# Kernel tuning notes

Hardware: AMD Instinct MI355X
Metric: run time of the kernel (lower is better)

Reference implementation:

```python
import jax, jax.numpy as jnp
import numpy as np
from jax.scipy.special import logsumexp

PAD_IDX, SOS_IDX, EOS_IDX = 0, 1, 2
NEG = -10000.0


def setup_inputs() -> dict:
    B, T, L = 64, 256, 8
    K, E, H = 128, 256, 512      # num_tags, EMBED_SIZE, HIDDEN_SIZE
    CV, WV = 128, 50000          # char / word vocab
    key = jax.random.key(0)
    ks = jax.random.split(key, 12)
    lengths = jax.random.randint(ks[0], (B,), T // 2, T + 1)
    mask = jnp.arange(T)[None, :] < lengths[:, None]          # [B,T] contiguous prefix
    wx = jnp.where(mask, jax.random.randint(ks[1], (B, T), 3, WV), 0).astype(jnp.int32)
    cx = jax.random.randint(ks[2], (B, T, L), 0, CV).astype(jnp.int32)
    y_body = jnp.where(mask, jax.random.randint(ks[3], (B, T), 3, K), PAD_IDX)
    y = jnp.concatenate([jnp.full((B, 1), SOS_IDX, jnp.int32), y_body.astype(jnp.int32)], 1)  # [B,T+1]
    s = 0.05
    char_emb = s * jax.random.normal(ks[4], (CV, E), jnp.float32)
    word_emb = s * jax.random.normal(ks[5], (WV, E), jnp.float32)
    Wi = s * jax.random.normal(ks[6], (E, 4 * H), jnp.float32)
    Wh = s * jax.random.normal(ks[7], (H, 4 * H), jnp.float32)
    b = jnp.zeros((4 * H,), jnp.float32)
    Wout = s * jax.random.normal(ks[8], (H, K), jnp.float32)
    bout = jnp.zeros((K,), jnp.float32)
    trans = jax.random.normal(ks[9], (K, K), jnp.float32)
    trans = trans.at[SOS_IDX, :].set(NEG)
    trans = trans.at[:, EOS_IDX].set(NEG)
    trans = trans.at[:, PAD_IDX].set(NEG)
    trans = trans.at[PAD_IDX, :].set(NEG)
    trans = trans.at[PAD_IDX, EOS_IDX].set(0.0)
    trans = trans.at[PAD_IDX, PAD_IDX].set(0.0)
    return dict(cx=cx, wx=wx, y=y, char_emb=char_emb, word_emb=word_emb,
                Wi=Wi, Wh=Wh, b=b, Wout=Wout, bout=bout, trans=trans)


def _forward(cx, wx, y, char_emb, word_emb, Wi, Wh, b, Wout, bout, trans):
    B, T = wx.shape
    K = trans.shape[0]
    H = Wh.shape[0]
    mask = (wx > 0)                                            # [B,T] bool
    maskf = mask.astype(jnp.float32)
    # embedding: word lookup + mean-pooled char lookup
    x = word_emb[wx] + char_emb[cx].mean(axis=2)               # [B,T,E]

    # masked LSTM (equivalent to pack_padded for prefix masks)
    def lstm_step(carry, inp):
        h, c = carry
        xt, mt = inp                                            # [B,E], [B,1]
        z = xt @ Wi + h @ Wh + b                                # [B,4H]
        i, f, g, o = jnp.split(z, 4, axis=-1)
        i, f, o = jax.nn.sigmoid(i), jax.nn.sigmoid(f), jax.nn.sigmoid(o)
        c_new = f * c + i * jnp.tanh(g)
        h_new = o * jnp.tanh(c_new)
        h = jnp.where(mt, h_new, h)
        c = jnp.where(mt, c_new, c)
        return (h, c), h

    h0 = jnp.zeros((B, H), x.dtype)
    xs = jnp.swapaxes(x, 0, 1)                                  # [T,B,E]
    ms = jnp.swapaxes(mask, 0, 1)[..., None]                    # [T,B,1]
    _, hs = jax.lax.scan(lstm_step, (h0, h0), (xs, ms))         # [T,B,H]
    hs = jnp.swapaxes(hs, 0, 1)                                 # [B,T,H]
    h = (hs @ Wout + bout) * maskf[..., None]                   # emissions [B,T,K]

    # CRF forward algorithm (log partition Z)
    score0 = jnp.full((B, K), NEG, h.dtype).at[:, SOS_IDX].set(0.0)

    def crf_step(score, inp):
        em, mt = inp                                            # [B,K], [B,1]
        s_t = logsumexp(score[:, None, :] + em[:, :, None] + trans[None, :, :], axis=-1)
        return jnp.where(mt, s_t, score), None

    emT = jnp.swapaxes(h, 0, 1)                                 # [T,B,K]
    scoreZ, _ = jax.lax.scan(crf_step, score0, (emT, ms))
    Z = logsumexp(scoreZ + trans[EOS_IDX], axis=-1)             # [B]

    # gold path score
    y_prev, y_next = y[:, :-1], y[:, 1:]                        # [B,T]
    emit = jnp.take_along_axis(h, y_next[..., None], axis=-1)[..., 0]  # [B,T]
    tr = trans[y_next, y_prev]                                  # [B,T]
    gold = jnp.sum((emit + tr) * maskf, axis=1)                 # [B]
    lengths = mask.sum(axis=1)
    last_tag = y[jnp.arange(B), lengths]                        # y has T+1 cols
    gold = gold + trans[EOS_IDX, last_tag]
    return Z - gold                                             # NLL per sequence [B]


def reference(cx, wx, y, char_emb, word_emb, Wi, Wh, b, Wout, bout, trans):
    return _forward(cx, wx, y, char_emb, word_emb, Wi, Wh, b, Wout, bout, trans)
```

## Files before the change

kernel.cpp:

```cpp
#include <hip/hip_runtime.h>


typedef float f32x4 __attribute__((ext_vector_type(4)));
typedef float f32x16 __attribute__((ext_vector_type(16)));
typedef __bf16 bf16x8 __attribute__((ext_vector_type(8)));
typedef unsigned int u32x4 __attribute__((ext_vector_type(4)));
typedef unsigned int u32x2 __attribute__((ext_vector_type(2)));

#define T_LEN 256
#define BB    64
#define EE    256
#define HH    512
#define KK    128
#define KCAT  768

static __device__ inline unsigned f2bf(float f) {
  union { float f; unsigned u; } v; v.f = f;
  unsigned r = v.u + 0x7FFF + ((v.u >> 16) & 1);
  return r >> 16;
}
static __device__ inline float sigm(float x) { return 1.f / (1.f + __expf(-x)); }
static __device__ inline float tanh_fast(float x) {
  return 1.f - 2.f / (1.f + __expf(2.f * x));
}
static __device__ inline bf16x8 ubf(u32x4 v) {
  union { u32x4 u; bf16x8 b; } c; c.u = v; return c.b;
}

__global__ __launch_bounds__(256) void build_wcat(
    const float* __restrict__ Wi, const float* __restrict__ Wh,
    unsigned short* __restrict__ WcatT) {
  __shared__ float tile[64][65];
  int ct = blockIdx.x & 31, kt = blockIdx.x >> 5;
  int tc = threadIdx.x & 63, tr = threadIdx.x >> 6;
  int c0 = ct * 64, k0 = kt * 64;
#pragma unroll
  for (int i = 0; i < 16; ++i) {
    int r = tr * 16 + i, k = k0 + r;
    float v = (k < EE) ? Wi[(size_t)k * 2048 + c0 + tc]
                       : Wh[(size_t)(k - EE) * 2048 + c0 + tc];
    tile[r][tc] = v;
  }
  __syncthreads();
#pragma unroll
  for (int i = 0; i < 16; ++i) {
    int cL = tr * 16 + i;
    WcatT[(size_t)(c0 + cL) * KCAT + k0 + tc] = (unsigned short)f2bf(tile[tc][cL]);
  }
}

__global__ __launch_bounds__(256) void build_wout(
    const float* __restrict__ Wout, unsigned short* __restrict__ WoutT) {
  __shared__ float tile[64][65];
  int ct = blockIdx.x & 1, kt = blockIdx.x >> 1;
  int tc = threadIdx.x & 63, tr = threadIdx.x >> 6;
  int c0 = ct * 64, k0 = kt * 64;
#pragma unroll
  for (int i = 0; i < 16; ++i) {
    int r = tr * 16 + i;
    tile[r][tc] = Wout[(size_t)(k0 + r) * KK + c0 + tc];
  }
  __syncthreads();
#pragma unroll
  for (int i = 0; i < 16; ++i) {
    int cL = tr * 16 + i;
    WoutT[(size_t)(c0 + cL) * HH + k0 + tc] = (unsigned short)f2bf(tile[tc][cL]);
  }
}

__global__ __launch_bounds__(256) void embed_kernel(
    const int* __restrict__ wx, const int* __restrict__ cx,
    const float* __restrict__ we, const float* __restrict__ ce,
    unsigned short* __restrict__ x) {
  int bid = blockIdx.x;
  int t = bid >> 6, b = bid & 63;
  int e = threadIdx.x;
  int w = wx[b * T_LEN + t];
  float v = we[(size_t)w * EE + e];
  const int* cp = cx + ((size_t)(b * T_LEN + t)) * 8;
  float s = 0.f;
#pragma unroll
  for (int l = 0; l < 8; ++l) s += ce[(size_t)cp[l] * EE + e];
  v += s * 0.125f;
  x[(size_t)bid * EE + e] = (unsigned short)f2bf(v);
}

__global__ void zero_flags(unsigned int* __restrict__ f) {
  unsigned z = 0u;
  asm volatile("global_store_dword %0, %1, off sc0 sc1"
               :: "v"(f + threadIdx.x), "v"(z) : "memory");
}

#define SBAR __builtin_amdgcn_sched_barrier(0)
#define WAITV(N) do { asm volatile("s_waitcnt vmcnt(" #N ")" ::: "memory"); SBAR; } while (0)
#define LDC(dst, ptr, OFF) \
  asm volatile("global_load_dwordx4 %0, %1, off offset:" OFF " sc0 sc1" \
               : "=v"(dst) : "v"(ptr) : "memory")
#define LDN(dst, ptr, OFF) \
  asm volatile("global_load_dwordx4 %0, %1, off offset:" OFF \
               : "=v"(dst) : "v"(ptr) : "memory")

#define ISSUE_X(B, P) do { \
  LDN(B[0],P,"0");   LDN(B[1],P,"32");  LDN(B[2],P,"64");  LDN(B[3],P,"96"); \
  LDN(B[4],P,"128"); LDN(B[5],P,"160"); LDN(B[6],P,"192"); LDN(B[7],P,"224"); \
  LDN(B[8],P,"256"); LDN(B[9],P,"288"); LDN(B[10],P,"320"); LDN(B[11],P,"352"); \
  LDN(B[12],P,"384"); LDN(B[13],P,"416"); LDN(B[14],P,"448"); LDN(B[15],P,"480"); } while (0)
#define ISSUE_H0(B, P) do { \
  LDC(B[0],P,"0");   LDC(B[1],P,"32");  LDC(B[2],P,"64");  LDC(B[3],P,"96"); \
  LDC(B[4],P,"128"); LDC(B[5],P,"160"); LDC(B[6],P,"192"); LDC(B[7],P,"224"); \
  LDC(B[8],P,"256"); LDC(B[9],P,"288"); LDC(B[10],P,"320"); LDC(B[11],P,"352"); \
  LDC(B[12],P,"384"); LDC(B[13],P,"416"); LDC(B[14],P,"448"); LDC(B[15],P,"480"); } while (0)
#define ISSUE_H1(B, P) do { \
  LDC(B[0],P,"512"); LDC(B[1],P,"544"); LDC(B[2],P,"576"); LDC(B[3],P,"608"); \
  LDC(B[4],P,"640"); LDC(B[5],P,"672"); LDC(B[6],P,"704"); LDC(B[7],P,"736"); \
  LDC(B[8],P,"768"); LDC(B[9],P,"800"); LDC(B[10],P,"832"); LDC(B[11],P,"864"); \
  LDC(B[12],P,"896"); LDC(B[13],P,"928"); LDC(B[14],P,"960"); LDC(B[15],P,"992"); } while (0)

#define GATES_STORE(T) do { \
    bool mk = ((int)wxv) > 0; \
    _Pragma("unroll") \
    for (int r = 0; r < 4; ++r) { \
      float zi = acc[r], zf = acc[4 + r], zg = acc[8 + r], zo = acc[12 + r]; \
      float cn = sigm(zf) * cst[r] + sigm(zi) * tanh_fast(zg); \
      float hn = sigm(zo) * tanh_fast(cn); \
      if (mk) { cst[r] = cn; hst[r] = hn; } \
    } \
    u32x2 ph; \
    ph[0] = f2bf(hst[0]) | (f2bf(hst[1]) << 16); \
    ph[1] = f2bf(hst[2]) | (f2bf(hst[3]) << 16); \
    asm volatile("global_store_dwordx2 %0, %1, off sc0 sc1" \
                 :: "v"(hstore + (size_t)(T) * 65536), "v"(ph) : "memory"); \
  } while (0)

__global__ __launch_bounds__(128, 1) void lstm_persistent(
    const unsigned short* __restrict__ x,
    unsigned short* __restrict__ hs,
    const unsigned short* __restrict__ WcatT,
    const float* __restrict__ bias,
    const int* __restrict__ wx,
    unsigned int* __restrict__ flags) {
  const int tid = threadIdx.x;
  const int lane = tid & 63;
  const int bhalf = tid >> 6;
  const int hi = lane >> 5;
  const int batch = bhalf * 32 + (lane & 31);
  const int u0 = blockIdx.x * 8;
  const int rr = lane & 31;
  const int wcol = (rr >> 3) * HH + u0 + (rr & 7);

  bf16x8 wreg[48];
#pragma unroll
  for (int kf = 0; kf < 48; ++kf)
    wreg[kf] = *(const bf16x8*)(WcatT + (size_t)wcol * KCAT + kf * 16 + hi * 8);

  float bv[16];
#pragma unroll
  for (int q = 0; q < 4; ++q)
#pragma unroll
    for (int r = 0; r < 4; ++r)
      bv[q * 4 + r] = bias[q * HH + u0 + 4 * hi + r];

  const char* xlane  = (const char*)x  + ((size_t)batch * EE + hi * 8) * 2;
  const char* hread  = (const char*)hs + ((size_t)batch * HH + hi * 8) * 2;
  char*       hstore = (char*)hs + ((size_t)batch * HH + u0 + 4 * hi) * 2;
  const int*  wxp    = wx + batch * T_LEN;

  float cst[4] = {0.f, 0.f, 0.f, 0.f};
  float hst[4] = {0.f, 0.f, 0.f, 0.f};
  u32x4 bufX[16], bufH[16];
  unsigned wxv;
  f32x16 acc;

  ISSUE_X(bufX, xlane);
  asm volatile("global_load_dword %0, %1, off" : "=v"(wxv) : "v"(wxp) : "memory");
  WAITV(0);
#pragma unroll
  for (int i = 0; i < 16; ++i) acc[i] = bv[i];
#pragma unroll
  for (int kf = 0; kf < 16; ++kf)
    acc = __builtin_amdgcn_mfma_f32_32x32x16_bf16(wreg[kf], ubf(bufX[kf]), acc, 0, 0, 0);
  GATES_STORE(0);
  WAITV(0);
  __syncthreads();
  if (tid == 0)
    __hip_atomic_store(flags + blockIdx.x, 1u, __ATOMIC_RELAXED, __HIP_MEMORY_SCOPE_AGENT);

  for (int t = 1; t < T_LEN; ++t) {
    const char* xt = xlane + (size_t)t * 32768;
    const char* hp = hread + (size_t)(t - 1) * 65536;

    ISSUE_X(bufX, xt);
    asm volatile("global_load_dword %0, %1, off" : "=v"(wxv) : "v"(wxp + t) : "memory");
    {
      unsigned v;
      do {
        asm volatile("global_load_dword %0, %1, off sc0 sc1\n\ts_waitcnt vmcnt(0)"
                     : "=v"(v) : "v"(flags + lane) : "memory");
      } while (!__all((int)(v >= (unsigned)t)));
      SBAR;
    }
    ISSUE_H0(bufH, hp);
#pragma unroll
    for (int i = 0; i < 16; ++i) acc[i] = bv[i];
#pragma unroll
    for (int kf = 0; kf < 16; ++kf)
      acc = __builtin_amdgcn_mfma_f32_32x32x16_bf16(wreg[kf], ubf(bufX[kf]), acc, 0, 0, 0);
    SBAR;
    ISSUE_H1(bufX, hp);
    WAITV(16);
#pragma unroll
    for (int kf = 0; kf < 16; ++kf)
      acc = __builtin_amdgcn_mfma_f32_32x32x16_bf16(wreg[16 + kf], ubf(bufH[kf]), acc, 0, 0, 0);
    WAITV(0);
#pragma unroll
    for (int kf = 0; kf < 16; ++kf)
      acc = __builtin_amdgcn_mfma_f32_32x32x16_bf16(wreg[32 + kf], ubf(bufX[kf]), acc, 0, 0, 0);
    GATES_STORE(t);
    WAITV(0);
    __syncthreads();
    if (tid == 0)
      __hip_atomic_store(flags + blockIdx.x, (unsigned)(t + 1),
                         __ATOMIC_RELAXED, __HIP_MEMORY_SCOPE_AGENT);
  }
}

__global__ __launch_bounds__(512) void em_gemm(
    const unsigned short* __restrict__ hs,
    const unsigned short* __restrict__ WoutT,
    const float* __restrict__ bout,
    const int* __restrict__ wx,
    float* __restrict__ em) {
  int mg = blockIdx.x;
  int wave = threadIdx.x >> 6, lane = threadIdx.x & 63;
  int m = wave >> 1, nh = wave & 1;
  int arow = lane & 15, kg = (lane >> 4) * 8;
  int rbase = mg * 64 + m * 16;
  const unsigned short* A = hs + (size_t)(rbase + arow) * HH + kg;
  f32x4 acc[4];
#pragma unroll
  for (int nt = 0; nt < 4; ++nt) acc[nt] = (f32x4){0.f, 0.f, 0.f, 0.f};
#pragma unroll
  for (int ks = 0; ks < 16; ++ks) {
    bf16x8 a = *(const bf16x8*)(A + ks * 32);
#pragma unroll
    for (int nt = 0; nt < 4; ++nt) {
      const unsigned short* Bp =
          WoutT + (size_t)(nh * 64 + nt * 16 + arow) * HH + kg + ks * 32;
      acc[nt] = __builtin_amdgcn_mfma_f32_16x16x32_bf16(a, *(const bf16x8*)Bp, acc[nt], 0, 0, 0);
    }
  }
#pragma unroll
  for (int nt = 0; nt < 4; ++nt) {
    int n = nh * 64 + nt * 16 + arow;
    float bo = bout[n];
#pragma unroll
    for (int r = 0; r < 4; ++r) {
      int row = rbase + (lane >> 4) * 4 + r;
      int t = row >> 6, b = row & 63;
      float v = (acc[nt][r] + bo) * ((wx[b * T_LEN + t] > 0) ? 1.f : 0.f);
      em[(size_t)row * KK + n] = v;
    }
  }
}

__global__ __launch_bounds__(512) void crf_kernel(
    const float* __restrict__ em,
    const float* __restrict__ trans,
    const int* __restrict__ wx,
    const int* __restrict__ y,
    float* __restrict__ out) {
  int b = blockIdx.x;
  __shared__ float tl[KK][129];
  __shared__ float sc[KK];
  __shared__ float red[512];
  __shared__ float red2[512];
  int tid = threadIdx.x;
  for (int i = tid; i < KK * KK; i += 512) tl[i >> 7][i & 127] = trans[i];
  if (tid < KK) sc[tid] = (tid == 1) ? 0.f : -10000.f;
  __syncthreads();

  int k = tid & 127, q = tid >> 7, j0 = q * 32;

  for (int t = 0; t < T_LEN; ++t) {
    if (wx[b * T_LEN + t] <= 0) continue;
    float mx = -1e30f;
#pragma unroll
    for (int j = 0; j < 32; ++j) mx = fmaxf(mx, sc[j0 + j] + tl[k][j0 + j]);
    float s = 0.f;
#pragma unroll
    for (int j = 0; j < 32; ++j) s += __expf(sc[j0 + j] + tl[k][j0 + j] - mx);
    red[tid] = mx; red2[tid] = s;
    __syncthreads();
    if (q == 0) {
      float M = mx, S = s;
#pragma unroll
      for (int qq = 1; qq < 4; ++qq) {
        float m2 = red[qq * 128 + k], s2 = red2[qq * 128 + k];
        float Mn = fmaxf(M, m2);
        S = S * __expf(M - Mn) + s2 * __expf(m2 - Mn);
        M = Mn;
      }
      sc[k] = em[(size_t)(t * BB + b) * KK + k] + M + __logf(S);
    }
    __syncthreads();
  }

  float term = 0.f, cnt = 0.f;
  if (tid < T_LEN) {
    int yp = y[b * 257 + tid], yn = y[b * 257 + tid + 1];
    if (wx[b * T_LEN + tid] > 0) {
      term = em[(size_t)(tid * BB + b) * KK + yn] + tl[yn][yp];
      cnt = 1.f;
    }
  }
  red[tid] = term; red2[tid] = cnt;
  __syncthreads();
  for (int s2 = 256; s2 > 0; s2 >>= 1) {
    if (tid < s2) { red[tid] += red[tid + s2]; red2[tid] += red2[tid + s2]; }
    __syncthreads();
  }
  float gold = red[0];
  int len = (int)(red2[0] + 0.5f);
  __syncthreads();

  float v = (tid < KK) ? sc[tid] + tl[2][tid] : -3.0e38f;
  red[tid] = v;
  __syncthreads();
  for (int s2 = 256; s2 > 0; s2 >>= 1) {
    if (tid < s2) red[tid] = fmaxf(red[tid], red[tid + s2]);
    __syncthreads();
  }
  float mz = red[0];
  __syncthreads();
  red[tid] = (tid < KK) ? __expf(v - mz) : 0.f;
  __syncthreads();
  for (int s2 = 256; s2 > 0; s2 >>= 1) {
    if (tid < s2) red[tid] += red[tid + s2];
    __syncthreads();
  }
  if (tid == 0) {
    float Z = mz + __logf(red[0]);
    int last_tag = y[b * 257 + len];
    out[b] = Z - (gold + tl[2][last_tag]);
  }
}

extern "C" void kernel_launch(void* const* d_in, const int* in_sizes, int n_in,
                              void* d_out, int out_size, void* d_ws, size_t ws_size,
                              hipStream_t stream) {
  const int*   cx    = (const int*)d_in[0];
  const int*   wx    = (const int*)d_in[1];
  const int*   y     = (const int*)d_in[2];
  const float* ce    = (const float*)d_in[3];
  const float* we    = (const float*)d_in[4];
  const float* Wi    = (const float*)d_in[5];
  const float* Wh    = (const float*)d_in[6];
  const float* bias  = (const float*)d_in[7];
  const float* Wout  = (const float*)d_in[8];
  const float* bout  = (const float*)d_in[9];
  const float* trans = (const float*)d_in[10];
  float* out = (float*)d_out;

  char* ws = (char*)d_ws;
  unsigned short* WcatT = (unsigned short*)(ws + 0);
  unsigned short* WoutT = (unsigned short*)(ws + 3145728);
  unsigned short* x     = (unsigned short*)(ws + 3276800);
  unsigned short* hs    = (unsigned short*)(ws + 11665408);
  unsigned int*   flags = (unsigned int*)(ws + 28442624);
  float*          em    = (float*)(ws + 3276800);

  build_wcat<<<384, 256, 0, stream>>>(Wi, Wh, WcatT);
  build_wout<<<16, 256, 0, stream>>>(Wout, WoutT);
  embed_kernel<<<T_LEN * BB, 256, 0, stream>>>(wx, cx, we, ce, x);
  zero_flags<<<1, 64, 0, stream>>>(flags);
  lstm_persistent<<<64, 128, 0, stream>>>(x, hs, WcatT, bias, wx, flags);
  em_gemm<<<256, 512, 0, stream>>>(hs, WoutT, bout, wx, em);
  crf_kernel<<<BB, 512, 0, stream>>>(em, trans, wx, y, out);
}
```

Baseline: 1.757 ms.

## Stream LSTM weights per step instead of register-resident, pad flags, precompute masks

The persistent LSTM kernel no longer keeps all 48 weight fragments in registers. It reloads them from global memory (L2) every timestep in 8-fragment double-buffered chunks, interleaved with the x and h loads and the MFMAs. Per-block flags are padded to separate 64-byte slots, only wave 0 polls (with s_sleep and an iteration cap), and the mask bits are precomputed into bitmasks. This relieves register pressure and polling contention, but adds per-step weight traffic on the serial critical path, and the poll cap could let a block proceed before the others are ready.

```diff
diff --git a/kernel.cpp b/kernel.cpp
--- a/kernel.cpp
+++ b/kernel.cpp
@@ -4,7 +4,6 @@
 typedef float f32x4 __attribute__((ext_vector_type(4)));
 typedef float f32x16 __attribute__((ext_vector_type(16)));
 typedef __bf16 bf16x8 __attribute__((ext_vector_type(8)));
-typedef unsigned int u32x4 __attribute__((ext_vector_type(4)));
 typedef unsigned int u32x2 __attribute__((ext_vector_type(2)));
 
 #define T_LEN 256
@@ -22,9 +21,6 @@
 static __device__ inline float sigm(float x) { return 1.f / (1.f + __expf(-x)); }
 static __device__ inline float tanh_fast(float x) {
   return 1.f - 2.f / (1.f + __expf(2.f * x));
-}
-static __device__ inline bf16x8 ubf(u32x4 v) {
-  union { u32x4 u; bf16x8 b; } c; c.u = v; return c.b;
 }
 
 __global__ __launch_bounds__(256) void build_wcat(
@@ -88,48 +84,29 @@
 __global__ void zero_flags(unsigned int* __restrict__ f) {
   unsigned z = 0u;
   asm volatile("global_store_dword %0, %1, off sc0 sc1"
-               :: "v"(f + threadIdx.x), "v"(z) : "memory");
+               :: "v"(f + blockIdx.x * 256 + threadIdx.x), "v"(z) : "memory");
 }
 
 #define SBAR __builtin_amdgcn_sched_barrier(0)
 #define WAITV(N) do { asm volatile("s_waitcnt vmcnt(" #N ")" ::: "memory"); SBAR; } while (0)
-#define LDC(dst, ptr, OFF) \
+#define LD(dst, p, OFF) \
+  asm volatile("global_load_dwordx4 %0, %1, off offset:" OFF \
+               : "=v"(dst) : "v"(p) : "memory")
+#define LS(dst, p, OFF) \
   asm volatile("global_load_dwordx4 %0, %1, off offset:" OFF " sc0 sc1" \
-               : "=v"(dst) : "v"(ptr) : "memory")
-#define LDN(dst, ptr, OFF) \
-  asm volatile("global_load_dwordx4 %0, %1, off offset:" OFF \
-               : "=v"(dst) : "v"(ptr) : "memory")
-
-#define ISSUE_X(B, P) do { \
-  LDN(B[0],P,"0");   LDN(B[1],P,"32");  LDN(B[2],P,"64");  LDN(B[3],P,"96"); \
-  LDN(B[4],P,"128"); LDN(B[5],P,"160"); LDN(B[6],P,"192"); LDN(B[7],P,"224"); \
-  LDN(B[8],P,"256"); LDN(B[9],P,"288"); LDN(B[10],P,"320"); LDN(B[11],P,"352"); \
-  LDN(B[12],P,"384"); LDN(B[13],P,"416"); LDN(B[14],P,"448"); LDN(B[15],P,"480"); } while (0)
-#define ISSUE_H0(B, P) do { \
-  LDC(B[0],P,"0");   LDC(B[1],P,"32");  LDC(B[2],P,"64");  LDC(B[3],P,"96"); \
-  LDC(B[4],P,"128"); LDC(B[5],P,"160"); LDC(B[6],P,"192"); LDC(B[7],P,"224"); \
-  LDC(B[8],P,"256"); LDC(B[9],P,"288"); LDC(B[10],P,"320"); LDC(B[11],P,"352"); \
-  LDC(B[12],P,"384"); LDC(B[13],P,"416"); LDC(B[14],P,"448"); LDC(B[15],P,"480"); } while (0)
-#define ISSUE_H1(B, P) do { \
-  LDC(B[0],P,"512"); LDC(B[1],P,"544"); LDC(B[2],P,"576"); LDC(B[3],P,"608"); \
-  LDC(B[4],P,"640"); LDC(B[5],P,"672"); LDC(B[6],P,"704"); LDC(B[7],P,"736"); \
-  LDC(B[8],P,"768"); LDC(B[9],P,"800"); LDC(B[10],P,"832"); LDC(B[11],P,"864"); \
-  LDC(B[12],P,"896"); LDC(B[13],P,"928"); LDC(B[14],P,"960"); LDC(B[15],P,"992"); } while (0)
-
-#define GATES_STORE(T) do { \
-    bool mk = ((int)wxv) > 0; \
-    _Pragma("unroll") \
-    for (int r = 0; r < 4; ++r) { \
-      float zi = acc[r], zf = acc[4 + r], zg = acc[8 + r], zo = acc[12 + r]; \
-      float cn = sigm(zf) * cst[r] + sigm(zi) * tanh_fast(zg); \
-      float hn = sigm(zo) * tanh_fast(cn); \
-      if (mk) { cst[r] = cn; hst[r] = hn; } \
-    } \
-    u32x2 ph; \
-    ph[0] = f2bf(hst[0]) | (f2bf(hst[1]) << 16); \
-    ph[1] = f2bf(hst[2]) | (f2bf(hst[3]) << 16); \
-    asm volatile("global_store_dwordx2 %0, %1, off sc0 sc1" \
-                 :: "v"(hstore + (size_t)(T) * 65536), "v"(ph) : "memory"); \
+               : "=v"(dst) : "v"(p) : "memory")
+
+#define IS_P8(B, P) do { \
+  LD(B[0],P,"0");   LD(B[1],P,"32");  LD(B[2],P,"64");  LD(B[3],P,"96"); \
+  LD(B[4],P,"128"); LD(B[5],P,"160"); LD(B[6],P,"192"); LD(B[7],P,"224"); } while (0)
+#define IS_S8(B, P) do { \
+  LS(B[0],P,"0");   LS(B[1],P,"32");  LS(B[2],P,"64");  LS(B[3],P,"96"); \
+  LS(B[4],P,"128"); LS(B[5],P,"160"); LS(B[6],P,"192"); LS(B[7],P,"224"); } while (0)
+
+#define MFMA8(W, D) do { \
+  _Pragma("unroll") \
+  for (int j_ = 0; j_ < 8; ++j_) \
+    acc = __builtin_amdgcn_mfma_f32_32x32x16_bf16(W[j_], D[j_], acc, 0, 0, 0); \
   } while (0)
 
 __global__ __launch_bounds__(128, 1) void lstm_persistent(
@@ -140,87 +117,103 @@
     const int* __restrict__ wx,
     unsigned int* __restrict__ flags) {
   const int tid = threadIdx.x;
-  const int lane = tid & 63;
-  const int bhalf = tid >> 6;
-  const int hi = lane >> 5;
-  const int batch = bhalf * 32 + (lane & 31);
+  const int wave = tid >> 6, lane = tid & 63;
+  const int hi2 = lane >> 5;
+  const int batch = wave * 32 + (lane & 31);
   const int u0 = blockIdx.x * 8;
   const int rr = lane & 31;
-  const int wcol = (rr >> 3) * HH + u0 + (rr & 7);
-
-  bf16x8 wreg[48];
-#pragma unroll
-  for (int kf = 0; kf < 48; ++kf)
-    wreg[kf] = *(const bf16x8*)(WcatT + (size_t)wcol * KCAT + kf * 16 + hi * 8);
+  const int col = (rr >> 3) * HH + u0 + (rr & 7);
+
+  const char* wbase = (const char*)WcatT + ((size_t)col * KCAT + hi2 * 8) * 2;
+  const char* xp    = (const char*)x + ((size_t)batch * EE + hi2 * 8) * 2;
+  const char* hp    = (const char*)hs + ((size_t)batch * HH + hi2 * 8) * 2;
+  char*       hstp  = (char*)hs + ((size_t)batch * HH + u0 + 4 * hi2) * 2;
+  unsigned int* myflag = flags + blockIdx.x * 16;
 
   float bv[16];
 #pragma unroll
-  for (int q = 0; q < 4; ++q)
-#pragma unroll
-    for (int r = 0; r < 4; ++r)
-      bv[q * 4 + r] = bias[q * HH + u0 + 4 * hi + r];
-
-  const char* xlane  = (const char*)x  + ((size_t)batch * EE + hi * 8) * 2;
-  const char* hread  = (const char*)hs + ((size_t)batch * HH + hi * 8) * 2;
-  char*       hstore = (char*)hs + ((size_t)batch * HH + u0 + 4 * hi) * 2;
-  const int*  wxp    = wx + batch * T_LEN;
-
-  float cst[4] = {0.f, 0.f, 0.f, 0.f};
-  float hst[4] = {0.f, 0.f, 0.f, 0.f};
-  u32x4 bufX[16], bufH[16];
-  unsigned wxv;
+  for (int g = 0; g < 4; ++g)
+#pragma unroll
+    for (int j = 0; j < 4; ++j) bv[g * 4 + j] = bias[g * HH + u0 + 4 * hi2 + j];
+
+  const int* wxp = wx + batch * T_LEN;
+  unsigned m8[8];
+#pragma unroll
+  for (int w8 = 0; w8 < 8; ++w8) {
+    unsigned m = 0;
+#pragma unroll
+    for (int k2 = 0; k2 < 32; ++k2)
+      m |= (wxp[w8 * 32 + k2] > 0) ? (1u << k2) : 0u;
+    m8[w8] = m;
+  }
+
+  float cst[4] = {0.f, 0.f, 0.f, 0.f}, hst[4] = {0.f, 0.f, 0.f, 0.f};
+  bf16x8 WA[8], DA[8], WB[8], DB[8];
   f32x16 acc;
 
-  ISSUE_X(bufX, xlane);
-  asm volatile("global_load_dword %0, %1, off" : "=v"(wxv) : "v"(wxp) : "memory");
-  WAITV(0);
-#pragma unroll
-  for (int i = 0; i < 16; ++i) acc[i] = bv[i];
-#pragma unroll
-  for (int kf = 0; kf < 16; ++kf)
-    acc = __builtin_amdgcn_mfma_f32_32x32x16_bf16(wreg[kf], ubf(bufX[kf]), acc, 0, 0, 0);
-  GATES_STORE(0);
-  WAITV(0);
-  __syncthreads();
-  if (tid == 0)
-    __hip_atomic_store(flags + blockIdx.x, 1u, __ATOMIC_RELAXED, __HIP_MEMORY_SCOPE_AGENT);
-
-  for (int t = 1; t < T_LEN; ++t) {
-    const char* xt = xlane + (size_t)t * 32768;
-    const char* hp = hread + (size_t)(t - 1) * 65536;
-
-    ISSUE_X(bufX, xt);
-    asm volatile("global_load_dword %0, %1, off" : "=v"(wxv) : "v"(wxp + t) : "memory");
-    {
-      unsigned v;
-      do {
-        asm volatile("global_load_dword %0, %1, off sc0 sc1\n\ts_waitcnt vmcnt(0)"
-                     : "=v"(v) : "v"(flags + lane) : "memory");
-      } while (!__all((int)(v >= (unsigned)t)));
-      SBAR;
-    }
-    ISSUE_H0(bufH, hp);
-#pragma unroll
-    for (int i = 0; i < 16; ++i) acc[i] = bv[i];
-#pragma unroll
-    for (int kf = 0; kf < 16; ++kf)
-      acc = __builtin_amdgcn_mfma_f32_32x32x16_bf16(wreg[kf], ubf(bufX[kf]), acc, 0, 0, 0);
-    SBAR;
-    ISSUE_H1(bufX, hp);
-    WAITV(16);
-#pragma unroll
-    for (int kf = 0; kf < 16; ++kf)
-      acc = __builtin_amdgcn_mfma_f32_32x32x16_bf16(wreg[16 + kf], ubf(bufH[kf]), acc, 0, 0, 0);
-    WAITV(0);
-#pragma unroll
-    for (int kf = 0; kf < 16; ++kf)
-      acc = __builtin_amdgcn_mfma_f32_32x32x16_bf16(wreg[32 + kf], ubf(bufX[kf]), acc, 0, 0, 0);
-    GATES_STORE(t);
-    WAITV(0);
-    __syncthreads();
-    if (tid == 0)
-      __hip_atomic_store(flags + blockIdx.x, (unsigned)(t + 1),
-                         __ATOMIC_RELAXED, __HIP_MEMORY_SCOPE_AGENT);
+#pragma unroll
+  for (int ph = 0; ph < 8; ++ph) {
+    const unsigned mw = m8[ph];
+#pragma unroll 1
+    for (int tt = 0; tt < 32; ++tt) {
+      const int t = ph * 32 + tt;
+      const bool mk = (mw >> tt) & 1u;
+
+      if (t > 0) {
+        if (wave == 0) {
+          unsigned v_; int it_ = 0;
+          for (;;) {
+            asm volatile("global_load_dword %0, %1, off sc0 sc1\n\ts_waitcnt vmcnt(0)"
+                         : "=v"(v_) : "v"(flags + lane * 16) : "memory");
+            if (__all((int)(v_ >= (unsigned)t))) break;
+            if (++it_ >= 65536) break;
+            __builtin_amdgcn_s_sleep(1);
+          }
+          SBAR;
+        }
+        __syncthreads();
+      }
+
+      const char* xt = xp + (size_t)t * 32768;
+      const char* ht = hp + (size_t)(t - 1) * 65536;
+
+      IS_P8(WA, wbase);         IS_P8(DA, xt);
+      IS_P8(WB, (wbase + 256)); IS_P8(DB, (xt + 256));
+#pragma unroll
+      for (int i = 0; i < 16; ++i) acc[i] = bv[i];
+      WAITV(16);  MFMA8(WA, DA);
+      if (t > 0) {
+        IS_P8(WA, (wbase + 512));  IS_S8(DA, ht);
+        WAITV(16);  MFMA8(WB, DB);
+        IS_P8(WB, (wbase + 768));  IS_S8(DB, (ht + 256));
+        WAITV(16);  MFMA8(WA, DA);
+        IS_P8(WA, (wbase + 1024)); IS_S8(DA, (ht + 512));
+        WAITV(16);  MFMA8(WB, DB);
+        IS_P8(WB, (wbase + 1280)); IS_S8(DB, (ht + 768));
+        WAITV(16);  MFMA8(WA, DA);
+        WAITV(0);   MFMA8(WB, DB);
+      } else {
+        WAITV(0);   MFMA8(WB, DB);
+      }
+
+#pragma unroll
+      for (int r = 0; r < 4; ++r) {
+        float zi = acc[r], zf = acc[4 + r], zg = acc[8 + r], zo = acc[12 + r];
+        float cn = sigm(zf) * cst[r] + sigm(zi) * tanh_fast(zg);
+        float hn = sigm(zo) * tanh_fast(cn);
+        if (mk) { cst[r] = cn; hst[r] = hn; }
+      }
+      u32x2 phh;
+      phh[0] = f2bf(hst[0]) | (f2bf(hst[1]) << 16);
+      phh[1] = f2bf(hst[2]) | (f2bf(hst[3]) << 16);
+      asm volatile("global_store_dwordx2 %0, %1, off sc0 sc1"
+                   :: "v"(hstp + (size_t)t * 65536), "v"(phh) : "memory");
+      WAITV(0);
+      __syncthreads();
+      if (tid == 0)
+        asm volatile("global_store_dword %0, %1, off sc0 sc1"
+                     :: "v"(myflag), "v"((unsigned)(t + 1)) : "memory");
+    }
   }
 }
 
@@ -372,7 +365,7 @@
   build_wcat<<<384, 256, 0, stream>>>(Wi, Wh, WcatT);
   build_wout<<<16, 256, 0, stream>>>(Wout, WoutT);
   embed_kernel<<<T_LEN * BB, 256, 0, stream>>>(wx, cx, we, ce, x);
-  zero_flags<<<1, 64, 0, stream>>>(flags);
+  zero_flags<<<4, 256, 0, stream>>>(flags);
   lstm_persistent<<<64, 128, 0, stream>>>(x, hs, WcatT, bias, wx, flags);
   em_gemm<<<256, 512, 0, stream>>>(hs, WoutT, bout, wx, em);
   crf_kernel<<<BB, 512, 0, stream>>>(em, trans, wx, y, out);
```

Result: slower. 2.358 ms (+34.2%).
